# Kernel optimization log

Measured on AMD Instinct MI355X. Metric: run time of the kernel, lower is better.

Reference implementation:

```python
import jax, jax.numpy as jnp
import numpy as np

G = 128          # number of point-cloud groups
DOWNSAMPLE = 256 # points per group
D = 256          # feature dim


def _pairwise_dist(x, y):
    # x: [G, n, d], y: [G, m, d] -> Euclidean distances [G, n, m]
    x2 = jnp.sum(x * x, axis=-1)[:, :, None]
    y2 = jnp.sum(y * y, axis=-1)[:, None, :]
    d2 = jnp.maximum(x2 + y2 - 2.0 * jnp.einsum('gnd,gmd->gnm', x, y), 0.0)
    # safe sqrt (zero diagonal has zero distance, avoid NaN grads)
    return jnp.where(d2 > 0, jnp.sqrt(jnp.where(d2 > 0, d2, 1.0)), 0.0)


def setup_inputs() -> dict:
    key = jax.random.key(0)
    k1, k2 = jax.random.split(key)
    inp = jax.random.normal(k1, (G * DOWNSAMPLE, D), dtype=jnp.float32)
    tgt = jax.random.normal(k2, (G * DOWNSAMPLE, D), dtype=jnp.float32)
    return {"input": inp, "target": tgt, "downsample": DOWNSAMPLE}


def reference(input, target, downsample):
    # MMDLoss.forward: reshape to (-1, downsample, D), batched energy distance, mean
    x = input.reshape(-1, downsample, input.shape[-1])   # [G, n, D]
    y = target.reshape(-1, downsample, target.shape[-1]) # [G, m, D]
    # Energy distance (geomloss 'energy' kernel k(x,y) = -||x-y||, uniform weights):
    # L = mean_ij ||x_i - y_j|| - 0.5 mean_ij ||x_i - x_j|| - 0.5 mean_ij ||y_i - y_j||
    d_xy = jnp.mean(_pairwise_dist(x, y), axis=(1, 2))  # [G]
    d_xx = jnp.mean(_pairwise_dist(x, x), axis=(1, 2))  # [G]
    d_yy = jnp.mean(_pairwise_dist(y, y), axis=(1, 2))  # [G]
    loss_per_group = d_xy - 0.5 * d_xx - 0.5 * d_yy
    return jnp.mean(loss_per_group)
```

## Files before the change

### kernel.cpp

```cpp
#include <hip/hip_runtime.h>
#include <hip/hip_bf16.h>
#include <stdint.h>
#include <string.h>

typedef __attribute__((ext_vector_type(8))) short short8;
typedef __attribute__((ext_vector_type(4))) float floatx4;

#define NPTS 256
#define DIM  256
#define TILE 128
#define BK   32
#define NIT  (DIM / BK)
#define LDSS 40

#define LDS_BARRIER() asm volatile("s_waitcnt lgkmcnt(0)\n\ts_barrier" ::: "memory")

static __device__ __forceinline__ uint32_t cvtsq2(float a, float b, float& s) {
    __hip_bfloat162 h = __float22bfloat162_rn(float2{a, b});
    uint32_t d;
    memcpy(&d, &h, 4);
    const float lo = __builtin_bit_cast(float, d << 16);
    const float hi = __builtin_bit_cast(float, d & 0xFFFF0000u);
    s += lo * lo + hi * hi;
    return d;
}
static __device__ __forceinline__ uint4 cvt8(const float4 u, const float4 v, float& s) {
    uint4 r;
    r.x = cvtsq2(u.x, u.y, s); r.y = cvtsq2(u.z, u.w, s);
    r.z = cvtsq2(v.x, v.y, s); r.w = cvtsq2(v.z, v.w, s);
    return r;
}

__global__ __launch_bounds__(512, 4)
void mmd_pipe(const float* __restrict__ X, const float* __restrict__ Y,
              float* __restrict__ out, float scale, int G) {
    int g, t;
    const int f = blockIdx.x;
    if ((G & 7) == 0) { const int xcd = f & 7, j = f >> 3; g = (j / 10) * 8 + xcd; t = j % 10; }
    else              { g = f / 10; t = f % 10; }

    int ptype, ti, tj; float w;
    if (t < 4)      { ptype = 0; ti = t >> 1; tj = t & 1; w = 1.0f; }
    else if (t < 7) { int u = t - 4; ptype = 1; ti = (u == 2); tj = (u >= 1); w = (u == 1) ? -1.0f : -0.5f; }
    else            { int u = t - 7; ptype = 2; ti = (u == 2); tj = (u >= 1); w = (u == 1) ? -1.0f : -0.5f; }

    const float *Pf, *Qf;
    if (ptype == 0)      { Pf = X; Qf = Y; }
    else if (ptype == 1) { Pf = X; Qf = X; }
    else                 { Pf = Y; Qf = Y; }
    const bool symdiag = (ptype != 0) && (ti == tj);

    const size_t prow0 = (size_t)g * NPTS + (size_t)ti * TILE;
    const size_t qrow0 = (size_t)g * NPTS + (size_t)tj * TILE;

    __shared__ __align__(16) uint16_t As[2][TILE * LDSS];
    __shared__ __align__(16) uint16_t Bs[2][TILE * LDSS];
    __shared__ float rnorm[TILE];
    __shared__ float cnorm[TILE];
    __shared__ float wpart[8];

    const int tid  = threadIdx.x;
    const int lane = tid & 63;
    const int wv   = tid >> 6;
    const int quad = lane >> 4;
    const int l15  = lane & 15;
    const int rowbase = (wv & 3) * 32;
    const int colbase = (wv >> 2) * 64;

    const int prow = tid >> 2;
    const int pcol = (tid & 3) * 8;
    const float* gA = Pf + (prow0 + prow) * DIM + pcol;
    const float* gB = Qf + (qrow0 + prow) * DIM + pcol;
    const int woff = prow * LDSS + pcol;

    floatx4 acc[2][4];
    #pragma unroll
    for (int i = 0; i < 2; ++i)
        #pragma unroll
        for (int j = 0; j < 4; ++j) acc[i][j] = (floatx4)0.0f;

    float sqp = 0.0f, sqq = 0.0f;

    float4 ra0 = *(const float4*)(gA);
    float4 ra1 = *(const float4*)(gA + 4);
    float4 rb0 = *(const float4*)(gB);
    float4 rb1 = *(const float4*)(gB + 4);
    {
        const uint4 pa = cvt8(ra0, ra1, sqp);
        const uint4 pb = cvt8(rb0, rb1, sqq);
        *(uint4*)&As[0][woff] = pa;
        *(uint4*)&Bs[0][woff] = pb;
    }
    ra0 = *(const float4*)(gA + BK);
    ra1 = *(const float4*)(gA + BK + 4);
    rb0 = *(const float4*)(gB + BK);
    rb1 = *(const float4*)(gB + BK + 4);

    #pragma unroll
    for (int it = 0; it < NIT; ++it) {
        const int b = it & 1;
        LDS_BARRIER();

        if (it < NIT - 1) {
            const uint4 pa = cvt8(ra0, ra1, sqp);
            const uint4 pb = cvt8(rb0, rb1, sqq);
            *(uint4*)&As[b ^ 1][woff] = pa;
            *(uint4*)&Bs[b ^ 1][woff] = pb;
        }
        if (it < NIT - 2) {
            const int k0 = (it + 2) * BK;
            ra0 = *(const float4*)(gA + k0);
            ra1 = *(const float4*)(gA + k0 + 4);
            rb0 = *(const float4*)(gB + k0);
            rb1 = *(const float4*)(gB + k0 + 4);
        }

        short8 af[2], bfr[4];
        #pragma unroll
        for (int mi = 0; mi < 2; ++mi)
            af[mi] = *(const short8*)&As[b][(rowbase + mi * 16 + l15) * LDSS + quad * 8];
        #pragma unroll
        for (int ni = 0; ni < 4; ++ni)
            bfr[ni] = *(const short8*)&Bs[b][(colbase + ni * 16 + l15) * LDSS + quad * 8];
        #pragma unroll
        for (int mi = 0; mi < 2; ++mi)
            #pragma unroll
            for (int ni = 0; ni < 4; ++ni)
                acc[mi][ni] = __builtin_amdgcn_mfma_f32_16x16x32_bf16(
                    af[mi], bfr[ni], acc[mi][ni], 0, 0, 0);
    }

    sqp += __shfl_xor(sqp, 1); sqp += __shfl_xor(sqp, 2);
    sqq += __shfl_xor(sqq, 1); sqq += __shfl_xor(sqq, 2);
    if ((tid & 3) == 0) { rnorm[prow] = sqp; cnorm[prow] = sqq; }
    __syncthreads();

    float lsum = 0.0f;
    #pragma unroll
    for (int mi = 0; mi < 2; ++mi) {
        #pragma unroll
        for (int i = 0; i < 4; ++i) {
            const int r = rowbase + mi * 16 + quad * 4 + i;
            const float rv = rnorm[r];
            #pragma unroll
            for (int ni = 0; ni < 4; ++ni) {
                const int c = colbase + ni * 16 + l15;
                float d2 = rv + cnorm[c] - 2.0f * acc[mi][ni][i];
                float s = sqrtf(fmaxf(d2, 0.0f));
                if (symdiag && (r == c)) s = 0.0f;
                lsum += s;
            }
        }
    }
    #pragma unroll
    for (int off = 32; off; off >>= 1) lsum += __shfl_down(lsum, off);
    if (lane == 0) wpart[wv] = lsum;
    __syncthreads();
    if (tid == 0) {
        float bs = 0.0f;
        #pragma unroll
        for (int i = 0; i < 8; ++i) bs += wpart[i];
        atomicAdd(out, bs * (w * scale));
    }
}

extern "C" void kernel_launch(void* const* d_in, const int* in_sizes, int n_in,
                              void* d_out, int out_size, void* d_ws, size_t ws_size,
                              hipStream_t stream) {
    const float* X = (const float*)d_in[0];
    const float* Y = (const float*)d_in[1];
    const int total_elems = in_sizes[0];
    const int G = total_elems / (NPTS * DIM);

    float* out = (float*)d_out;
    hipMemsetAsync(out, 0, sizeof(float) * out_size, stream);

    const float scale = 1.0f / ((float)NPTS * (float)NPTS * (float)G);
    mmd_pipe<<<10 * G, 512, 0, stream>>>(X, Y, out, scale, G);
}
```

Before: 123.2 us.

## Split into bf16 pre-convert kernel and LDS-free direct-load MFMA GEMM

Adds a pre-pass kernel that converts X and Y to bf16 once and computes per-row squared norms into workspace. A new GEMM kernel then loads bf16 fragments straight from global memory into MFMA operands, with no LDS staging and no barriers, using 4 waves each computing a 64x64 sub-tile. This removes the repeated fp32 loads and conversions that happened in every one of the 10 tile blocks per group, and it halves the bytes read. The cost is an extra launch, a workspace round trip, and uncoalesced short8 global loads that depend on L2 hits. The old fused kernel is kept as a fallback when the workspace is too small.

```diff
diff --git a/kernel.cpp b/kernel.cpp
--- a/kernel.cpp
+++ b/kernel.cpp
@@ -9,11 +9,7 @@
 #define NPTS 256
 #define DIM  256
 #define TILE 128
-#define BK   32
-#define NIT  (DIM / BK)
-#define LDSS 40
-
-#define LDS_BARRIER() asm volatile("s_waitcnt lgkmcnt(0)\n\ts_barrier" ::: "memory")
+#define NIT  8
 
 static __device__ __forceinline__ uint32_t cvtsq2(float a, float b, float& s) {
     __hip_bfloat162 h = __float22bfloat162_rn(float2{a, b});
@@ -24,13 +20,136 @@
     s += lo * lo + hi * hi;
     return d;
 }
+
+__global__ __launch_bounds__(256)
+void mmd_cvt(const float* __restrict__ X, const float* __restrict__ Y,
+             float* __restrict__ x2, float* __restrict__ y2,
+             uint16_t* __restrict__ Xb, uint16_t* __restrict__ Yb, int npts) {
+    const int lane = threadIdx.x & 63;
+    const int wv   = threadIdx.x >> 6;
+    const int pblk = blockIdx.x * 16;
+    #pragma unroll
+    for (int r = 0; r < 4; ++r) {
+        const int p = pblk + wv + 4 * r;
+        const float* src; float* dst; uint16_t* bdst; int pl;
+        if (p < npts) { src = X; dst = x2; bdst = Xb; pl = p; }
+        else          { src = Y; dst = y2; bdst = Yb; pl = p - npts; }
+        const float4 v = *(const float4*)(src + (size_t)pl * DIM + lane * 4);
+        float ssq = 0.0f;
+        uint2 pk;
+        pk.x = cvtsq2(v.x, v.y, ssq);
+        pk.y = cvtsq2(v.z, v.w, ssq);
+        *(uint2*)(bdst + (size_t)pl * DIM + lane * 4) = pk;
+        #pragma unroll
+        for (int off = 32; off; off >>= 1) ssq += __shfl_down(ssq, off);
+        if (lane == 0) dst[pl] = ssq;
+    }
+}
+
+__global__ __launch_bounds__(256, 4)
+void mmd_gemm(const uint16_t* __restrict__ Xb, const uint16_t* __restrict__ Yb,
+              const float* __restrict__ x2, const float* __restrict__ y2,
+              float* __restrict__ out, float scale, int G) {
+    int g, t;
+    const int f = blockIdx.x;
+    if ((G & 7) == 0) { const int xcd = f & 7, j = f >> 3; g = (j / 10) * 8 + xcd; t = j % 10; }
+    else              { g = f / 10; t = f % 10; }
+
+    int ptype, ti, tj; float w;
+    if (t < 4)      { ptype = 0; ti = t >> 1; tj = t & 1; w = 1.0f; }
+    else if (t < 7) { int u = t - 4; ptype = 1; ti = (u == 2); tj = (u >= 1); w = (u == 1) ? -1.0f : -0.5f; }
+    else            { int u = t - 7; ptype = 2; ti = (u == 2); tj = (u >= 1); w = (u == 1) ? -1.0f : -0.5f; }
+
+    const uint16_t *Pb, *Qb; const float *rn_g, *cn_g;
+    if (ptype == 0)      { Pb = Xb; Qb = Yb; rn_g = x2; cn_g = y2; }
+    else if (ptype == 1) { Pb = Xb; Qb = Xb; rn_g = x2; cn_g = x2; }
+    else                 { Pb = Yb; Qb = Yb; rn_g = y2; cn_g = y2; }
+    const bool symdiag = (ptype != 0) && (ti == tj);
+
+    const size_t prow0 = (size_t)g * NPTS + (size_t)ti * TILE;
+    const size_t qrow0 = (size_t)g * NPTS + (size_t)tj * TILE;
+
+    const int tid  = threadIdx.x;
+    const int lane = tid & 63;
+    const int wv   = tid >> 6;
+    const int wrow = (wv >> 1) * 64;
+    const int wcol = (wv & 1) * 64;
+    const int quad = lane >> 4;
+    const int l15  = lane & 15;
+
+    const uint16_t* pa[4];
+    const uint16_t* pb[4];
+    #pragma unroll
+    for (int mi = 0; mi < 4; ++mi)
+        pa[mi] = Pb + (prow0 + wrow + mi * 16 + l15) * DIM + quad * 8;
+    #pragma unroll
+    for (int ni = 0; ni < 4; ++ni)
+        pb[ni] = Qb + (qrow0 + wcol + ni * 16 + l15) * DIM + quad * 8;
+
+    floatx4 acc[4][4];
+    #pragma unroll
+    for (int i = 0; i < 4; ++i)
+        #pragma unroll
+        for (int j = 0; j < 4; ++j) acc[i][j] = (floatx4)0.0f;
+
+    #pragma unroll
+    for (int it = 0; it < NIT; ++it) {
+        const int k0 = it * 32;
+        short8 af[4], bfr[4];
+        #pragma unroll
+        for (int mi = 0; mi < 4; ++mi) af[mi]  = *(const short8*)(pa[mi] + k0);
+        #pragma unroll
+        for (int ni = 0; ni < 4; ++ni) bfr[ni] = *(const short8*)(pb[ni] + k0);
+        #pragma unroll
+        for (int mi = 0; mi < 4; ++mi)
+            #pragma unroll
+            for (int ni = 0; ni < 4; ++ni)
+                acc[mi][ni] = __builtin_amdgcn_mfma_f32_16x16x32_bf16(
+                    af[mi], bfr[ni], acc[mi][ni], 0, 0, 0);
+    }
+
+    float cn[4];
+    #pragma unroll
+    for (int ni = 0; ni < 4; ++ni) cn[ni] = cn_g[qrow0 + wcol + ni * 16 + l15];
+
+    float lsum = 0.0f;
+    #pragma unroll
+    for (int mi = 0; mi < 4; ++mi) {
+        #pragma unroll
+        for (int i = 0; i < 4; ++i) {
+            const int r = wrow + mi * 16 + quad * 4 + i;
+            const float rv = rn_g[prow0 + r];
+            #pragma unroll
+            for (int ni = 0; ni < 4; ++ni) {
+                const int c = wcol + ni * 16 + l15;
+                float d2 = rv + cn[ni] - 2.0f * acc[mi][ni][i];
+                float s = sqrtf(fmaxf(d2, 0.0f));
+                if (symdiag && (r == c)) s = 0.0f;
+                lsum += s;
+            }
+        }
+    }
+    #pragma unroll
+    for (int off = 32; off; off >>= 1) lsum += __shfl_down(lsum, off);
+
+    __shared__ float wpart[4];
+    if (lane == 0) wpart[wv] = lsum;
+    __syncthreads();
+    if (tid == 0) {
+        const float bs = wpart[0] + wpart[1] + wpart[2] + wpart[3];
+        atomicAdd(out, bs * (w * scale));
+    }
+}
+
+#define BK   32
+#define LDSS 40
+#define LDS_BARRIER() asm volatile("s_waitcnt lgkmcnt(0)\n\ts_barrier" ::: "memory")
 static __device__ __forceinline__ uint4 cvt8(const float4 u, const float4 v, float& s) {
     uint4 r;
     r.x = cvtsq2(u.x, u.y, s); r.y = cvtsq2(u.z, u.w, s);
     r.z = cvtsq2(v.x, v.y, s); r.w = cvtsq2(v.z, v.w, s);
     return r;
 }
-
 __global__ __launch_bounds__(512, 4)
 void mmd_pipe(const float* __restrict__ X, const float* __restrict__ Y,
               float* __restrict__ out, float scale, int G) {
@@ -38,83 +157,52 @@
     const int f = blockIdx.x;
     if ((G & 7) == 0) { const int xcd = f & 7, j = f >> 3; g = (j / 10) * 8 + xcd; t = j % 10; }
     else              { g = f / 10; t = f % 10; }
-
     int ptype, ti, tj; float w;
     if (t < 4)      { ptype = 0; ti = t >> 1; tj = t & 1; w = 1.0f; }
     else if (t < 7) { int u = t - 4; ptype = 1; ti = (u == 2); tj = (u >= 1); w = (u == 1) ? -1.0f : -0.5f; }
     else            { int u = t - 7; ptype = 2; ti = (u == 2); tj = (u >= 1); w = (u == 1) ? -1.0f : -0.5f; }
-
     const float *Pf, *Qf;
     if (ptype == 0)      { Pf = X; Qf = Y; }
     else if (ptype == 1) { Pf = X; Qf = X; }
     else                 { Pf = Y; Qf = Y; }
     const bool symdiag = (ptype != 0) && (ti == tj);
-
     const size_t prow0 = (size_t)g * NPTS + (size_t)ti * TILE;
     const size_t qrow0 = (size_t)g * NPTS + (size_t)tj * TILE;
-
     __shared__ __align__(16) uint16_t As[2][TILE * LDSS];
     __shared__ __align__(16) uint16_t Bs[2][TILE * LDSS];
-    __shared__ float rnorm[TILE];
-    __shared__ float cnorm[TILE];
-    __shared__ float wpart[8];
-
-    const int tid  = threadIdx.x;
-    const int lane = tid & 63;
-    const int wv   = tid >> 6;
-    const int quad = lane >> 4;
-    const int l15  = lane & 15;
-    const int rowbase = (wv & 3) * 32;
-    const int colbase = (wv >> 2) * 64;
-
-    const int prow = tid >> 2;
-    const int pcol = (tid & 3) * 8;
+    __shared__ float rnorm[TILE]; __shared__ float cnorm[TILE]; __shared__ float wpart[8];
+    const int tid = threadIdx.x, lane = tid & 63, wv = tid >> 6;
+    const int quad = lane >> 4, l15 = lane & 15;
+    const int rowbase = (wv & 3) * 32, colbase = (wv >> 2) * 64;
+    const int prow = tid >> 2, pcol = (tid & 3) * 8;
     const float* gA = Pf + (prow0 + prow) * DIM + pcol;
     const float* gB = Qf + (qrow0 + prow) * DIM + pcol;
     const int woff = prow * LDSS + pcol;
-
     floatx4 acc[2][4];
     #pragma unroll
     for (int i = 0; i < 2; ++i)
         #pragma unroll
         for (int j = 0; j < 4; ++j) acc[i][j] = (floatx4)0.0f;
-
     float sqp = 0.0f, sqq = 0.0f;
-
-    float4 ra0 = *(const float4*)(gA);
-    float4 ra1 = *(const float4*)(gA + 4);
-    float4 rb0 = *(const float4*)(gB);
-    float4 rb1 = *(const float4*)(gB + 4);
-    {
-        const uint4 pa = cvt8(ra0, ra1, sqp);
-        const uint4 pb = cvt8(rb0, rb1, sqq);
-        *(uint4*)&As[0][woff] = pa;
-        *(uint4*)&Bs[0][woff] = pb;
-    }
-    ra0 = *(const float4*)(gA + BK);
-    ra1 = *(const float4*)(gA + BK + 4);
-    rb0 = *(const float4*)(gB + BK);
-    rb1 = *(const float4*)(gB + BK + 4);
-
-    #pragma unroll
-    for (int it = 0; it < NIT; ++it) {
+    float4 ra0 = *(const float4*)(gA), ra1 = *(const float4*)(gA + 4);
+    float4 rb0 = *(const float4*)(gB), rb1 = *(const float4*)(gB + 4);
+    { const uint4 pa = cvt8(ra0, ra1, sqp); const uint4 pb = cvt8(rb0, rb1, sqq);
+      *(uint4*)&As[0][woff] = pa; *(uint4*)&Bs[0][woff] = pb; }
+    ra0 = *(const float4*)(gA + BK); ra1 = *(const float4*)(gA + BK + 4);
+    rb0 = *(const float4*)(gB + BK); rb1 = *(const float4*)(gB + BK + 4);
+    #pragma unroll
+    for (int it = 0; it < DIM / BK; ++it) {
         const int b = it & 1;
         LDS_BARRIER();
-
-        if (it < NIT - 1) {
-            const uint4 pa = cvt8(ra0, ra1, sqp);
-            const uint4 pb = cvt8(rb0, rb1, sqq);
-            *(uint4*)&As[b ^ 1][woff] = pa;
-            *(uint4*)&Bs[b ^ 1][woff] = pb;
-        }
-        if (it < NIT - 2) {
+        if (it < DIM / BK - 1) {
+            const uint4 pa = cvt8(ra0, ra1, sqp); const uint4 pb = cvt8(rb0, rb1, sqq);
+            *(uint4*)&As[b ^ 1][woff] = pa; *(uint4*)&Bs[b ^ 1][woff] = pb;
+        }
+        if (it < DIM / BK - 2) {
             const int k0 = (it + 2) * BK;
-            ra0 = *(const float4*)(gA + k0);
-            ra1 = *(const float4*)(gA + k0 + 4);
-            rb0 = *(const float4*)(gB + k0);
-            rb1 = *(const float4*)(gB + k0 + 4);
-        }
-
+            ra0 = *(const float4*)(gA + k0); ra1 = *(const float4*)(gA + k0 + 4);
+            rb0 = *(const float4*)(gB + k0); rb1 = *(const float4*)(gB + k0 + 4);
+        }
         short8 af[2], bfr[4];
         #pragma unroll
         for (int mi = 0; mi < 2; ++mi)
@@ -129,15 +217,13 @@
                 acc[mi][ni] = __builtin_amdgcn_mfma_f32_16x16x32_bf16(
                     af[mi], bfr[ni], acc[mi][ni], 0, 0, 0);
     }
-
     sqp += __shfl_xor(sqp, 1); sqp += __shfl_xor(sqp, 2);
     sqq += __shfl_xor(sqq, 1); sqq += __shfl_xor(sqq, 2);
     if ((tid & 3) == 0) { rnorm[prow] = sqp; cnorm[prow] = sqq; }
     __syncthreads();
-
     float lsum = 0.0f;
     #pragma unroll
-    for (int mi = 0; mi < 2; ++mi) {
+    for (int mi = 0; mi < 2; ++mi)
         #pragma unroll
         for (int i = 0; i < 4; ++i) {
             const int r = rowbase + mi * 16 + quad * 4 + i;
@@ -151,7 +237,6 @@
                 lsum += s;
             }
         }
-    }
     #pragma unroll
     for (int off = 32; off; off >>= 1) lsum += __shfl_down(lsum, off);
     if (lane == 0) wpart[wv] = lsum;
@@ -170,11 +255,24 @@
     const float* X = (const float*)d_in[0];
     const float* Y = (const float*)d_in[1];
     const int total_elems = in_sizes[0];
-    const int G = total_elems / (NPTS * DIM);
+    const int npts = total_elems / DIM;
+    const int G = npts / NPTS;
 
     float* out = (float*)d_out;
     hipMemsetAsync(out, 0, sizeof(float) * out_size, stream);
-
     const float scale = 1.0f / ((float)NPTS * (float)NPTS * (float)G);
-    mmd_pipe<<<10 * G, 512, 0, stream>>>(X, Y, out, scale, G);
-}
+
+    float* x2 = (float*)d_ws;
+    float* y2 = x2 + npts;
+    uint16_t* Xb = (uint16_t*)(y2 + npts);
+    uint16_t* Yb = Xb + (size_t)total_elems;
+    const size_t need = (size_t)npts * 2 * sizeof(float)
+                      + (size_t)total_elems * 2 * sizeof(uint16_t);
+
+    if (ws_size >= need) {
+        mmd_cvt<<<(2 * npts) / 16, 256, 0, stream>>>(X, Y, x2, y2, Xb, Yb, npts);
+        mmd_gemm<<<10 * G, 256, 0, stream>>>(Xb, Yb, x2, y2, out, scale, G);
+    } else {
+        mmd_pipe<<<10 * G, 512, 0, stream>>>(X, Y, out, scale, G);
+    }
+}
```

New measurement: 154.4 us. 1.25x slower.

## Double K-tile to 64 and restructure global load, convert, and store pipeline

Applied to the files above, without the earlier changes.

Raises the K step from 32 to 64, which halves the number of barrier iterations and runs two MFMA sub-steps per tile. Each thread now loads four 16-byte float4 chunks from rows spaced 32 apart, in place of two adjacent float4s. The bf16 conversion and LDS store now happen after the MFMAs, so global loads for the next tile overlap with the math. It also drops the min-blocks-per-CU launch bound. The trade-off is twice the LDS per block and more live registers, which may lower occupancy, and a longer shuffle reduction for the row norms.

```diff
diff --git a/kernel.cpp b/kernel.cpp
--- a/kernel.cpp
+++ b/kernel.cpp
@@ -9,9 +9,9 @@
 #define NPTS 256
 #define DIM  256
 #define TILE 128
-#define BK   32
+#define BK   64
 #define NIT  (DIM / BK)
-#define LDSS 40
+#define LDSS 72
 
 #define LDS_BARRIER() asm volatile("s_waitcnt lgkmcnt(0)\n\ts_barrier" ::: "memory")
 
@@ -24,14 +24,8 @@
     s += lo * lo + hi * hi;
     return d;
 }
-static __device__ __forceinline__ uint4 cvt8(const float4 u, const float4 v, float& s) {
-    uint4 r;
-    r.x = cvtsq2(u.x, u.y, s); r.y = cvtsq2(u.z, u.w, s);
-    r.z = cvtsq2(v.x, v.y, s); r.w = cvtsq2(v.z, v.w, s);
-    return r;
-}
-
-__global__ __launch_bounds__(512, 4)
+
+__global__ __launch_bounds__(512)
 void mmd_pipe(const float* __restrict__ X, const float* __restrict__ Y,
               float* __restrict__ out, float scale, int G) {
     int g, t;
@@ -67,11 +61,11 @@
     const int rowbase = (wv & 3) * 32;
     const int colbase = (wv >> 2) * 64;
 
-    const int prow = tid >> 2;
-    const int pcol = (tid & 3) * 8;
-    const float* gA = Pf + (prow0 + prow) * DIM + pcol;
-    const float* gB = Qf + (qrow0 + prow) * DIM + pcol;
-    const int woff = prow * LDSS + pcol;
+    const int trow = tid >> 4;
+    const int tcol = (tid & 15) * 4;
+    const float* gA = Pf + (prow0 + trow) * DIM + tcol;
+    const float* gB = Qf + (qrow0 + trow) * DIM + tcol;
+    const int woff = trow * LDSS + tcol;
 
     floatx4 acc[2][4];
     #pragma unroll
@@ -79,22 +73,26 @@
         #pragma unroll
         for (int j = 0; j < 4; ++j) acc[i][j] = (floatx4)0.0f;
 
-    float sqp = 0.0f, sqq = 0.0f;
-
-    float4 ra0 = *(const float4*)(gA);
-    float4 ra1 = *(const float4*)(gA + 4);
-    float4 rb0 = *(const float4*)(gB);
-    float4 rb1 = *(const float4*)(gB + 4);
-    {
-        const uint4 pa = cvt8(ra0, ra1, sqp);
-        const uint4 pb = cvt8(rb0, rb1, sqq);
-        *(uint4*)&As[0][woff] = pa;
-        *(uint4*)&Bs[0][woff] = pb;
-    }
-    ra0 = *(const float4*)(gA + BK);
-    ra1 = *(const float4*)(gA + BK + 4);
-    rb0 = *(const float4*)(gB + BK);
-    rb1 = *(const float4*)(gB + BK + 4);
+    float sqa[4] = {0.f, 0.f, 0.f, 0.f};
+    float sqb[4] = {0.f, 0.f, 0.f, 0.f};
+
+    float4 ra[4], rb[4];
+
+    #pragma unroll
+    for (int p = 0; p < 4; ++p) {
+        ra[p] = *(const float4*)(gA + p * (32 * DIM));
+        rb[p] = *(const float4*)(gB + p * (32 * DIM));
+    }
+    #pragma unroll
+    for (int p = 0; p < 4; ++p) {
+        uint2 wa, wb;
+        wa.x = cvtsq2(ra[p].x, ra[p].y, sqa[p]);
+        wa.y = cvtsq2(ra[p].z, ra[p].w, sqa[p]);
+        wb.x = cvtsq2(rb[p].x, rb[p].y, sqb[p]);
+        wb.y = cvtsq2(rb[p].z, rb[p].w, sqb[p]);
+        *(uint2*)&As[0][woff + p * (32 * LDSS)] = wa;
+        *(uint2*)&Bs[0][woff + p * (32 * LDSS)] = wb;
+    }
 
     #pragma unroll
     for (int it = 0; it < NIT; ++it) {
@@ -102,37 +100,61 @@
         LDS_BARRIER();
 
         if (it < NIT - 1) {
-            const uint4 pa = cvt8(ra0, ra1, sqp);
-            const uint4 pb = cvt8(rb0, rb1, sqq);
-            *(uint4*)&As[b ^ 1][woff] = pa;
-            *(uint4*)&Bs[b ^ 1][woff] = pb;
-        }
-        if (it < NIT - 2) {
-            const int k0 = (it + 2) * BK;
-            ra0 = *(const float4*)(gA + k0);
-            ra1 = *(const float4*)(gA + k0 + 4);
-            rb0 = *(const float4*)(gB + k0);
-            rb1 = *(const float4*)(gB + k0 + 4);
-        }
-
-        short8 af[2], bfr[4];
-        #pragma unroll
-        for (int mi = 0; mi < 2; ++mi)
-            af[mi] = *(const short8*)&As[b][(rowbase + mi * 16 + l15) * LDSS + quad * 8];
-        #pragma unroll
-        for (int ni = 0; ni < 4; ++ni)
-            bfr[ni] = *(const short8*)&Bs[b][(colbase + ni * 16 + l15) * LDSS + quad * 8];
-        #pragma unroll
-        for (int mi = 0; mi < 2; ++mi)
+            const int kk = (it + 1) * BK;
+            #pragma unroll
+            for (int p = 0; p < 4; ++p) {
+                ra[p] = *(const float4*)(gA + kk + p * (32 * DIM));
+                rb[p] = *(const float4*)(gB + kk + p * (32 * DIM));
+            }
+        }
+
+        #pragma unroll
+        for (int ks = 0; ks < 2; ++ks) {
+            const int kof = ks * 32 + quad * 8;
+            short8 af[2], bfr[4];
+            #pragma unroll
+            for (int mi = 0; mi < 2; ++mi)
+                af[mi] = *(const short8*)&As[b][(rowbase + mi * 16 + l15) * LDSS + kof];
             #pragma unroll
             for (int ni = 0; ni < 4; ++ni)
-                acc[mi][ni] = __builtin_amdgcn_mfma_f32_16x16x32_bf16(
-                    af[mi], bfr[ni], acc[mi][ni], 0, 0, 0);
-    }
-
-    sqp += __shfl_xor(sqp, 1); sqp += __shfl_xor(sqp, 2);
-    sqq += __shfl_xor(sqq, 1); sqq += __shfl_xor(sqq, 2);
-    if ((tid & 3) == 0) { rnorm[prow] = sqp; cnorm[prow] = sqq; }
+                bfr[ni] = *(const short8*)&Bs[b][(colbase + ni * 16 + l15) * LDSS + kof];
+            #pragma unroll
+            for (int mi = 0; mi < 2; ++mi)
+                #pragma unroll
+                for (int ni = 0; ni < 4; ++ni)
+                    acc[mi][ni] = __builtin_amdgcn_mfma_f32_16x16x32_bf16(
+                        af[mi], bfr[ni], acc[mi][ni], 0, 0, 0);
+        }
+
+        if (it < NIT - 1) {
+            #pragma unroll
+            for (int p = 0; p < 4; ++p) {
+                uint2 wa, wb;
+                wa.x = cvtsq2(ra[p].x, ra[p].y, sqa[p]);
+                wa.y = cvtsq2(ra[p].z, ra[p].w, sqa[p]);
+                wb.x = cvtsq2(rb[p].x, rb[p].y, sqb[p]);
+                wb.y = cvtsq2(rb[p].z, rb[p].w, sqb[p]);
+                *(uint2*)&As[b ^ 1][woff + p * (32 * LDSS)] = wa;
+                *(uint2*)&Bs[b ^ 1][woff + p * (32 * LDSS)] = wb;
+            }
+        }
+    }
+
+    #pragma unroll
+    for (int p = 0; p < 4; ++p) {
+        #pragma unroll
+        for (int m = 1; m < 16; m <<= 1) {
+            sqa[p] += __shfl_xor(sqa[p], m);
+            sqb[p] += __shfl_xor(sqb[p], m);
+        }
+    }
+    if ((tid & 15) == 0) {
+        #pragma unroll
+        for (int p = 0; p < 4; ++p) {
+            rnorm[trow + 32 * p] = sqa[p];
+            cnorm[trow + 32 * p] = sqb[p];
+        }
+    }
     __syncthreads();
 
     float lsum = 0.0f;
```

Result: slower. 131.9 us (+7.1%).
